# Kernel tuning notes

Measured on AMD Instinct MI355X. Metric: run time of the kernel, lower is better.

## Reference

```python
import jax, jax.numpy as jnp
import numpy as np

B, S, DMAX, NMEL, DM, K = 8, 100, 12, 80, 128, 9
T = S * DMAX  # 1200 max mel frames
EPS = 1e-5  # BatchNorm eps (eval mode, running_mean=0, running_var=1)


def setup_inputs() -> dict:
    key = jax.random.key(0)
    ks = jax.random.split(key, 16)
    durations = jax.random.randint(ks[0], (B, S), 4, DMAX + 1).astype(jnp.int32)
    mel_len = jnp.sum(durations, axis=1).astype(jnp.int32)
    src_len = jnp.full((B,), S, dtype=jnp.int32)
    mel = jax.random.normal(ks[1], (B, T, NMEL), dtype=jnp.float32)
    # conv stack params (xavier-ish uniform)
    s1 = float(np.sqrt(6.0 / (1 * K + DM * K)))
    w1 = jax.random.uniform(ks[2], (DM, 1, 1, K), minval=-s1, maxval=s1, dtype=jnp.float32)
    g1 = 1.0 + 0.1 * jax.random.normal(ks[3], (DM,), dtype=jnp.float32)
    be1 = 0.1 * jax.random.normal(ks[4], (DM,), dtype=jnp.float32)
    s2 = float(np.sqrt(6.0 / (DM * K + 1 * K)))
    w2 = jax.random.uniform(ks[5], (1, DM, 1, K), minval=-s2, maxval=s2, dtype=jnp.float32)
    g2 = 1.0 + 0.1 * jax.random.normal(ks[6], (1,), dtype=jnp.float32)
    be2 = 0.1 * jax.random.normal(ks[7], (1,), dtype=jnp.float32)
    # BiGRU params (pytorch layout: gates [r|z|n] stacked -> 3*H rows)
    sh = float(1.0 / np.sqrt(DM))
    u = lambda k, shape: jax.random.uniform(k, shape, minval=-sh, maxval=sh, dtype=jnp.float32)
    w_ih_f = u(ks[8], (3 * DM, NMEL)); w_hh_f = u(ks[9], (3 * DM, DM))
    b_ih_f = u(ks[10], (3 * DM,));    b_hh_f = u(ks[11], (3 * DM,))
    w_ih_b = u(ks[12], (3 * DM, NMEL)); w_hh_b = u(ks[13], (3 * DM, DM))
    b_ih_b = u(ks[14], (3 * DM,));    b_hh_b = u(ks[15], (3 * DM,))
    return {"mel": mel, "durations": durations, "mel_len": mel_len, "src_len": src_len,
            "w1": w1, "g1": g1, "be1": be1, "w2": w2, "g2": g2, "be2": be2,
            "w_ih_f": w_ih_f, "w_hh_f": w_hh_f, "b_ih_f": b_ih_f, "b_hh_f": b_hh_f,
            "w_ih_b": w_ih_b, "w_hh_b": w_hh_b, "b_ih_b": b_ih_b, "b_hh_b": b_hh_b}


def _bn_eval(x, g, b):
    # eval-mode BatchNorm2d with running_mean=0, running_var=1; x [B,C,T,M]
    scale = g / jnp.sqrt(1.0 + EPS)
    return x * scale[None, :, None, None] + b[None, :, None, None]


def _gru_scan(xs_seq, reset_seq, w_hh, b_hh):
    # xs_seq [T,B,3H] precomputed input projections; reset_seq [T,B] 1.0 -> reset h to 0
    H = w_hh.shape[1]
    Bn = xs_seq.shape[1]

    def step(h, inp):
        xg, rst = inp
        h = h * (1.0 - rst)[:, None]
        hg = h @ w_hh.T + b_hh
        xr, xz, xn = jnp.split(xg, 3, axis=-1)
        hr, hz, hn = jnp.split(hg, 3, axis=-1)
        r = jax.nn.sigmoid(xr + hr)
        z = jax.nn.sigmoid(xz + hz)
        n = jnp.tanh(xn + r * hn)
        h_new = (1.0 - z) * n + z * h
        return h_new, h_new

    h0 = jnp.zeros((Bn, H), xs_seq.dtype)
    _, hs = jax.lax.scan(step, h0, (xs_seq, reset_seq))
    return hs  # [T,B,H]


def reference(mel, durations, mel_len, src_len, w1, g1, be1, w2, g2, be2,
              w_ih_f, w_hh_f, b_ih_f, b_hh_f, w_ih_b, w_hh_b, b_ih_b, b_hh_b):
    pad = (K - 1) // 2
    # conv stack: kernel (1,K) mixes only the mel-channel axis -> apply to full mel once
    x = mel[:, None, :, :]  # [B,1,T,M]
    x = jax.lax.conv_general_dilated(x, w1, (1, 1), [(0, 0), (pad, pad)])
    x = jax.nn.relu(_bn_eval(x, g1, be1))
    x = jax.lax.conv_general_dilated(x, w2, (1, 1), [(0, 0), (pad, pad)])
    x = jax.nn.relu(_bn_eval(x, g2, be2))
    x = x[:, 0]  # [B,T,M]

    # segment boundaries from durations (all phones valid here, durations > 0)
    cum = jnp.cumsum(durations, axis=1)      # [B,S]
    starts = cum - durations                 # segment start frame per phone
    ends = cum - 1                           # segment end frame per phone
    bidx = jnp.arange(B)[:, None]
    start_mask = jnp.zeros((B, T), x.dtype).at[bidx, starts].set(1.0)
    end_mask = jnp.zeros((B, T), x.dtype).at[bidx, ends].set(1.0)

    # forward direction: reset h at segment starts, read h at segment ends
    xf = jnp.einsum('btm,gm->tbg', x, w_ih_f) + b_ih_f
    Hf = _gru_scan(xf, start_mask.T, w_hh_f, b_hh_f)           # [T,B,H]
    # backward direction: scan reversed time, reset at original segment ends
    xb = jnp.einsum('btm,gm->tbg', x, w_ih_b) + b_ih_b
    Hb = _gru_scan(xb[::-1], end_mask.T[::-1], w_hh_b, b_hh_b)[::-1]  # [T,B,H], orig time

    hf = jnp.take_along_axis(jnp.transpose(Hf, (1, 0, 2)), ends[..., None], axis=1)    # [B,S,H]
    hb = jnp.take_along_axis(jnp.transpose(Hb, (1, 0, 2)), starts[..., None], axis=1)  # [B,S,H]
    out = jnp.concatenate([hf, hb], axis=-1)  # [B,S,2H]
    valid = (jnp.arange(S)[None, :] < src_len[:, None])[..., None]
    return jnp.where(valid, out, 0.0)
```

## Files before the change

kernel.cpp:

```cpp
#include <hip/hip_runtime.h>
#include <math.h>

#define BB   8
#define SS   100
#define TT   1200
#define NM   80
#define DMC  128
#define KK   9
#define G3   384
#define NROW (BB*TT)

typedef __attribute__((ext_vector_type(8))) short short8;
typedef __attribute__((ext_vector_type(4))) float f32x4;

__device__ __forceinline__ float sigmoid_(float v) { return 1.f / (1.f + __expf(-v)); }
__device__ __forceinline__ float tanh_(float v) {
    float a = fabsf(v);
    float e = __expf(-2.f * a);
    float t = (1.f - e) / (1.f + e);
    return copysignf(t, v);
}
__device__ __forceinline__ unsigned short f2bf(float f) {
    unsigned int u = __float_as_uint(f);
    unsigned int r = (u + 0x7fffu + ((u >> 16) & 1u)) >> 16;
    return (unsigned short)r;
}

__global__ __launch_bounds__(1024) void k_prep(
    const float* __restrict__ whf, const float* __restrict__ whb,
    const float* __restrict__ wif, const float* __restrict__ wib,
    const float* __restrict__ bf, const float* __restrict__ bbv,
    const int* __restrict__ dur,
    unsigned short* __restrict__ wph, unsigned short* __restrict__ wpl,
    unsigned short* __restrict__ wih_h, unsigned short* __restrict__ wih_l,
    float* __restrict__ biasc, int* __restrict__ starts) {
    int blk = blockIdx.x;
    int tid = threadIdx.x;
    if (blk < 12) {
        int idx = blk * 1024 + tid;
        int lane = idx & 63;
        int k32  = (idx >> 6) & 3;
        int tau  = (idx >> 8) % 24;
        int dir  = idx / (24 * 4 * 64);
        const float* w = dir ? whb : whf;
        int g = tau * 16 + (lane & 15);
        int kbase = k32 * 32 + (lane >> 4) * 8;
#pragma unroll
        for (int j = 0; j < 8; j++) {
            float v = w[g * DMC + kbase + j];
            unsigned short hi = f2bf(v);
            float hif = __uint_as_float(((unsigned)hi) << 16);
            unsigned short lo = f2bf(v - hif);
            wph[idx * 8 + j] = hi;
            wpl[idx * 8 + j] = lo;
        }
    } else if (blk < 21) {
        int idx = (blk - 12) * 1024 + tid;
        int lane = idx & 63;
        int ks   = (idx >> 6) % 3;
        int tau  = idx / (3 * 64);
        int gate = tau * 16 + (lane & 15);
        int kb   = ks * 32 + (lane >> 4) * 8;
        const float* w = (gate < G3) ? (wif + gate * NM) : (wib + (gate - G3) * NM);
#pragma unroll
        for (int j = 0; j < 8; j++) {
            int k = kb + j;
            float v = (k < NM) ? w[k] : 0.f;
            unsigned short hi = f2bf(v);
            float hif = __uint_as_float(((unsigned)hi) << 16);
            unsigned short lo = f2bf(v - hif);
            wih_h[idx * 8 + j] = hi;
            wih_l[idx * 8 + j] = lo;
        }
    } else {
        __shared__ int buf[BB][128];
        int s = tid & 127, b = tid >> 7;
        int v = (s < SS) ? dur[b * SS + s] : 0;
        buf[b][s] = v;
        __syncthreads();
        for (int off = 1; off < 128; off <<= 1) {
            int t = (s >= off) ? buf[b][s - off] : 0;
            __syncthreads();
            buf[b][s] += t;
            __syncthreads();
        }
        if (s < SS) starts[b * SS + s] = buf[b][s] - v;
        if (tid < 768) biasc[tid] = (tid < G3) ? bf[tid] : bbv[tid - G3];
    }
}

__global__ __launch_bounds__(256) void k_conv(
    const float* __restrict__ mel, const int* __restrict__ mel_len,
    const float* __restrict__ w1, const float* __restrict__ g1, const float* __restrict__ be1,
    const float* __restrict__ w2, const float* __restrict__ g2, const float* __restrict__ be2,
    float* __restrict__ xout) {
    int b = blockIdx.y;
    int t = blockIdx.x;
    int ml = mel_len[b];
    if (t >= ml) return;

    __shared__ __align__(16) float mp[96];
    __shared__ __align__(16) float part[8][84];

    int tid = threadIdx.x;
    int mq = tid >> 6, g = tid & 63;
    int ms = 20 * mq;
    const float inv_sqrt = 0.9999950000374997f;

    if (tid < 96) {
        float v = 0.f;
        if (tid >= 8 && tid < 88) v = mel[(b * TT + t) * NM + tid - 8];
        mp[tid] = v;
    }
    __syncthreads();

    float c[20];
#pragma unroll
    for (int m = 0; m < 20; m++) c[m] = 0.f;

#pragma unroll 1
    for (int dd = 0; dd < 2; dd++) {
        int d = g + 64 * dd;
        float sc = g1[d] * inv_sqrt;
        float w1r[KK], w2r[KK];
#pragma unroll
        for (int k = 0; k < KK; k++) { w1r[k] = w1[d * KK + k] * sc; w2r[k] = w2[d * KK + k]; }
        float sb = be1[d];

        float mw[12];
        {
            const float4* p4 = (const float4*)(mp + ms);
            float4 a = p4[0], bq = p4[1], cq = p4[2];
            mw[0]=a.x;  mw[1]=a.y;  mw[2]=a.z;  mw[3]=a.w;
            mw[4]=bq.x; mw[5]=bq.y; mw[6]=bq.z; mw[7]=bq.w;
            mw[8]=cq.x; mw[9]=cq.y; mw[10]=cq.z; mw[11]=cq.w;
        }
#pragma unroll
        for (int ch = 0; ch < 7; ch++) {
#pragma unroll
            for (int jj = 0; jj < 4; jj++) {
                int off = ch * 4 + jj;
                float yv = sb;
#pragma unroll
                for (int k = 0; k < KK; k++) yv = fmaf(w1r[k], mw[jj + k], yv);
                yv = fmaxf(yv, 0.f);
                int j = ms + off;
                if (j < 4 || j >= 84) yv = 0.f;
#pragma unroll
                for (int k = 0; k < KK; k++) {
                    int mo = off - k;
                    if (mo >= 0 && mo < 20) c[mo] = fmaf(w2r[k], yv, c[mo]);
                }
            }
            if (ch < 6) {
#pragma unroll
                for (int q = 0; q < 8; q++) mw[q] = mw[q + 4];
                const float4* p4 = (const float4*)(mp + ms + ch * 4 + 12);
                float4 a = p4[0];
                mw[8]=a.x; mw[9]=a.y; mw[10]=a.z; mw[11]=a.w;
            }
        }
    }

#pragma unroll
    for (int m = 0; m < 20; m++) {
        c[m] += __shfl_xor(c[m], 1);
        c[m] += __shfl_xor(c[m], 2);
        c[m] += __shfl_xor(c[m], 4);
    }
    if ((g & 7) == 0) {
        int p = g >> 3;
#pragma unroll
        for (int m = 0; m < 20; m += 4)
            *(float4*)&part[p][ms + m] = make_float4(c[m], c[m+1], c[m+2], c[m+3]);
    }
    __syncthreads();

    if (tid < 80) {
        float s = 0.f;
#pragma unroll
        for (int p = 0; p < 8; p++) s += part[p][tid];
        float v = fmaxf(0.f, fmaf(s, g2[0] * inv_sqrt, be2[0]));
        xout[(b * TT + t) * NM + tid] = v;
    }
}

__global__ __launch_bounds__(512, 2) void k_gru(
    const float* __restrict__ x,
    const unsigned short* __restrict__ wph, const unsigned short* __restrict__ wpl,
    const unsigned short* __restrict__ wih_h, const unsigned short* __restrict__ wih_l,
    const float* __restrict__ biasc,
    const int* __restrict__ dur_all, const int* __restrict__ starts,
    const int* __restrict__ src_len,
    const float* __restrict__ bhf, const float* __restrict__ bhb,
    float* __restrict__ out) {
    int sblk = blockIdx.x;
    int b    = blockIdx.y;
    int dir  = blockIdx.z;
    int s0 = sblk * 16;

    __shared__ __align__(16) unsigned short hbh[2][2048];
    __shared__ __align__(16) unsigned short hbl[2][2048];
    __shared__ __align__(16) short8 xbh[2][192];
    __shared__ __align__(16) short8 xbl[2][192];
    __shared__ int sdur[16], sstart[16];

    int tid  = threadIdx.x;
    int wave = tid >> 6, lane = tid & 63;
    int quad = lane >> 4, seg = lane & 15;

    if (tid < 16) {
        int ss = s0 + tid;
        sdur[tid]   = (ss < SS) ? dur_all[b * SS + ss] : 0;
        sstart[tid] = (ss < SS) ? starts[b * SS + ss]  : 0;
    }
    for (int i = tid; i < 2048; i += 512) { hbh[0][i] = 0; hbl[0][i] = 0; }

    short8 Ah[3][4], Al[3][4];
    const short8* wph8 = (const short8*)wph;
    const short8* wpl8 = (const short8*)wpl;
#pragma unroll
    for (int tt = 0; tt < 3; tt++)
#pragma unroll
        for (int k32 = 0; k32 < 4; k32++) {
            int idx = ((dir * 24 + wave + 8 * tt) * 4 + k32) * 64 + lane;
            Ah[tt][k32] = wph8[idx];
            Al[tt][k32] = wpl8[idx];
        }
    short8 Gh[3][3], Gl[3][3];
    const short8* wih_h8 = (const short8*)wih_h;
    const short8* wih_l8 = (const short8*)wih_l;
#pragma unroll
    for (int tt = 0; tt < 3; tt++)
#pragma unroll
        for (int ks = 0; ks < 3; ks++) {
            int idx = ((dir * 24 + wave + 8 * tt) * 3 + ks) * 64 + lane;
            Gh[tt][ks] = wih_h8[idx];
            Gl[tt][ks] = wih_l8[idx];
        }

    int s = s0 + seg;
    int sd = (s < SS) ? dur_all[b * SS + s] : 0;
    int st = (s < SS) ? starts[b * SS + s]  : 0;
    int slb = src_len[b];
    const float* bih = biasc + dir * G3;
    const float* bhh = dir ? bhb : bhf;
    int j0 = wave * 16 + quad * 4;
    float4 i_r = *(const float4*)&bih[j0];
    float4 i_z = *(const float4*)&bih[DMC + j0];
    float4 bxn = *(const float4*)&bih[2 * DMC + j0];
    float4 h_r = *(const float4*)&bhh[j0];
    float4 h_z = *(const float4*)&bhh[DMC + j0];
    float4 bhn = *(const float4*)&bhh[2 * DMC + j0];
    float4 br = make_float4(i_r.x + h_r.x, i_r.y + h_r.y, i_r.z + h_r.z, i_r.w + h_r.w);
    float4 bz = make_float4(i_z.x + h_z.x, i_z.y + h_z.y, i_z.z + h_z.z, i_z.w + h_z.w);
    float4 h = make_float4(0.f, 0.f, 0.f, 0.f);

    int idx8 = (j0 >> 5) * 64 + ((j0 >> 3) & 3) * 16 + seg;
    int wbase = idx8 * 8 + (j0 & 7);

    __syncthreads();

    if (tid < 192) {
        int ks = tid >> 6, ln = tid & 63;
        int sg = ln & 15, qq = ln >> 4;
        int kb = ks * 32 + qq * 8;
        short8 hi8 = {0,0,0,0,0,0,0,0}, lo8 = {0,0,0,0,0,0,0,0};
        if (kb < NM && 0 < sdur[sg]) {
            int t = dir ? (sstart[sg] + sdur[sg] - 1) : sstart[sg];
            const float* xr = x + (size_t)(b * TT + t) * NM + kb;
#pragma unroll
            for (int j = 0; j < 8; j++) {
                float v = xr[j];
                unsigned short hi = f2bf(v);
                hi8[j] = (short)hi;
                lo8[j] = (short)f2bf(v - __uint_as_float(((unsigned)hi) << 16));
            }
        }
        xbh[0][tid] = hi8;
        xbl[0][tid] = lo8;
    }
    __syncthreads();

    for (int i = 0; i < 12; i++) {
        int p = i & 1;
        bool act = (i < sd);

        f32x4 acc0 = (f32x4){0.f,0.f,0.f,0.f};
        f32x4 acc1 = (f32x4){0.f,0.f,0.f,0.f};
        f32x4 acc2 = (f32x4){0.f,0.f,0.f,0.f};
        f32x4 acc3 = (f32x4){0.f,0.f,0.f,0.f};
#pragma unroll
        for (int ks = 0; ks < 3; ks++) {
            short8 Bxh = xbh[p][ks * 64 + lane];
            short8 Bxl = xbl[p][ks * 64 + lane];
            acc0 = __builtin_amdgcn_mfma_f32_16x16x32_bf16(Gh[0][ks], Bxh, acc0, 0, 0, 0);
            acc0 = __builtin_amdgcn_mfma_f32_16x16x32_bf16(Gh[0][ks], Bxl, acc0, 0, 0, 0);
            acc0 = __builtin_amdgcn_mfma_f32_16x16x32_bf16(Gl[0][ks], Bxh, acc0, 0, 0, 0);
            acc1 = __builtin_amdgcn_mfma_f32_16x16x32_bf16(Gh[1][ks], Bxh, acc1, 0, 0, 0);
            acc1 = __builtin_amdgcn_mfma_f32_16x16x32_bf16(Gh[1][ks], Bxl, acc1, 0, 0, 0);
            acc1 = __builtin_amdgcn_mfma_f32_16x16x32_bf16(Gl[1][ks], Bxh, acc1, 0, 0, 0);
            acc3 = __builtin_amdgcn_mfma_f32_16x16x32_bf16(Gh[2][ks], Bxh, acc3, 0, 0, 0);
            acc3 = __builtin_amdgcn_mfma_f32_16x16x32_bf16(Gh[2][ks], Bxl, acc3, 0, 0, 0);
            acc3 = __builtin_amdgcn_mfma_f32_16x16x32_bf16(Gl[2][ks], Bxh, acc3, 0, 0, 0);
        }
#pragma unroll
        for (int k32 = 0; k32 < 4; k32++) {
            short8 Bh = ((const short8*)hbh[p])[k32 * 64 + lane];
            short8 Bl = ((const short8*)hbl[p])[k32 * 64 + lane];
            acc0 = __builtin_amdgcn_mfma_f32_16x16x32_bf16(Ah[0][k32], Bh, acc0, 0, 0, 0);
            acc0 = __builtin_amdgcn_mfma_f32_16x16x32_bf16(Ah[0][k32], Bl, acc0, 0, 0, 0);
            acc0 = __builtin_amdgcn_mfma_f32_16x16x32_bf16(Al[0][k32], Bh, acc0, 0, 0, 0);
            acc1 = __builtin_amdgcn_mfma_f32_16x16x32_bf16(Ah[1][k32], Bh, acc1, 0, 0, 0);
            acc1 = __builtin_amdgcn_mfma_f32_16x16x32_bf16(Ah[1][k32], Bl, acc1, 0, 0, 0);
            acc1 = __builtin_amdgcn_mfma_f32_16x16x32_bf16(Al[1][k32], Bh, acc1, 0, 0, 0);
            acc2 = __builtin_amdgcn_mfma_f32_16x16x32_bf16(Ah[2][k32], Bh, acc2, 0, 0, 0);
            acc2 = __builtin_amdgcn_mfma_f32_16x16x32_bf16(Ah[2][k32], Bl, acc2, 0, 0, 0);
            acc2 = __builtin_amdgcn_mfma_f32_16x16x32_bf16(Al[2][k32], Bh, acc2, 0, 0, 0);
        }

        if (act) {
            float hv[4]  = {h.x, h.y, h.z, h.w};
            float brv[4] = {br.x, br.y, br.z, br.w};
            float bzv[4] = {bz.x, bz.y, bz.z, bz.w};
            float bxv[4] = {bxn.x, bxn.y, bxn.z, bxn.w};
            float bhv[4] = {bhn.x, bhn.y, bhn.z, bhn.w};
#pragma unroll
            for (int cmp = 0; cmp < 4; cmp++) {
                float r = sigmoid_(acc0[cmp] + brv[cmp]);
                float z = sigmoid_(acc1[cmp] + bzv[cmp]);
                float n = tanh_(acc3[cmp] + bxv[cmp] + r * (acc2[cmp] + bhv[cmp]));
                hv[cmp] = (1.f - z) * n + z * hv[cmp];
            }
            h = make_float4(hv[0], hv[1], hv[2], hv[3]);
            if (i == sd - 1) {
                float4 vout = (s < slb) ? h : make_float4(0.f, 0.f, 0.f, 0.f);
                *(float4*)&out[(b * SS + s) * (2 * DMC) + dir * DMC + j0] = vout;
            }
        }

        {
            float hv[4] = {h.x, h.y, h.z, h.w};
            unsigned short hs_[4], ls_[4];
#pragma unroll
            for (int cmp = 0; cmp < 4; cmp++) {
                unsigned short hi = f2bf(hv[cmp]);
                float hif = __uint_as_float(((unsigned)hi) << 16);
                hs_[cmp] = hi;
                ls_[cmp] = f2bf(hv[cmp] - hif);
            }
            *(ushort4*)&hbh[1 - p][wbase] = make_ushort4(hs_[0], hs_[1], hs_[2], hs_[3]);
            *(ushort4*)&hbl[1 - p][wbase] = make_ushort4(ls_[0], ls_[1], ls_[2], ls_[3]);
        }

        if (tid < 192) {
            int i2 = i + 1;
            int ks = tid >> 6, ln = tid & 63;
            int sg = ln & 15, qq = ln >> 4;
            int kb = ks * 32 + qq * 8;
            short8 hi8 = {0,0,0,0,0,0,0,0}, lo8 = {0,0,0,0,0,0,0,0};
            int d2 = sdur[sg];
            if (kb < NM && i2 < d2) {
                int t = dir ? (sstart[sg] + d2 - 1 - i2) : (sstart[sg] + i2);
                const float* xr = x + (size_t)(b * TT + t) * NM + kb;
#pragma unroll
                for (int j = 0; j < 8; j++) {
                    float v = xr[j];
                    unsigned short hi = f2bf(v);
                    hi8[j] = (short)hi;
                    lo8[j] = (short)f2bf(v - __uint_as_float(((unsigned)hi) << 16));
                }
            }
            xbh[1 - p][tid] = hi8;
            xbl[1 - p][tid] = lo8;
        }
        __syncthreads();
    }
}

extern "C" void kernel_launch(void* const* d_in, const int* in_sizes, int n_in,
                              void* d_out, int out_size, void* d_ws, size_t ws_size,
                              hipStream_t stream) {
    const float* mel      = (const float*)d_in[0];
    const int*   durations= (const int*)  d_in[1];
    const int*   mel_len  = (const int*)  d_in[2];
    const int*   src_len  = (const int*)  d_in[3];
    const float* w1       = (const float*)d_in[4];
    const float* g1       = (const float*)d_in[5];
    const float* be1      = (const float*)d_in[6];
    const float* w2       = (const float*)d_in[7];
    const float* g2       = (const float*)d_in[8];
    const float* be2      = (const float*)d_in[9];
    const float* w_ih_f   = (const float*)d_in[10];
    const float* w_hh_f   = (const float*)d_in[11];
    const float* b_ih_f   = (const float*)d_in[12];
    const float* b_hh_f   = (const float*)d_in[13];
    const float* w_ih_b   = (const float*)d_in[14];
    const float* w_hh_b   = (const float*)d_in[15];
    const float* b_ih_b   = (const float*)d_in[16];
    const float* b_hh_b   = (const float*)d_in[17];
    float* out = (float*)d_out;

    float* x    = (float*)d_ws;
    unsigned short* wph   = (unsigned short*)(x + NROW * NM);
    unsigned short* wpl   = wph + 2 * 24 * 4 * 64 * 8;
    unsigned short* wih_h = wpl + 2 * 24 * 4 * 64 * 8;
    unsigned short* wih_l = wih_h + 48 * 3 * 64 * 8;
    float* biasc = (float*)(wih_l + 48 * 3 * 64 * 8);
    int*   starts= (int*)(biasc + 768);

    k_prep<<<22, 1024, 0, stream>>>(w_hh_f, w_hh_b, w_ih_f, w_ih_b, b_ih_f, b_ih_b,
                                    durations, wph, wpl, wih_h, wih_l, biasc, starts);
    k_conv<<<dim3(TT, BB), 256, 0, stream>>>(mel, mel_len, w1, g1, be1, w2, g2, be2, x);
    k_gru<<<dim3(7, 8, 2), 512, 0, stream>>>(x, wph, wpl, wih_h, wih_l, biasc,
                                             durations, starts, src_len,
                                             b_hh_f, b_hh_b, out);
}
```

Measured before the change: 166.9 us.

## Pair conv frames with packed FMA and preload all GRU inputs upfront

The conv kernel now handles two time frames per block and uses v_pk_fma_f32 on interleaved float pairs, which halves the block count and shares weight loads between the two frames. The GRU kernel now converts all 12 steps' input vectors to bf16 hi/lo in shared memory before the recurrence starts. This removes the per-step global load and conversion from the serial loop. The x and h projections also go into separate accumulators, which shortens the MFMA dependency chains. The cost is more shared memory per GRU block, which may lower occupancy, and a longer prologue.

```diff
diff --git a/kernel.cpp b/kernel.cpp
--- a/kernel.cpp
+++ b/kernel.cpp
@@ -12,6 +12,7 @@
 
 typedef __attribute__((ext_vector_type(8))) short short8;
 typedef __attribute__((ext_vector_type(4))) float f32x4;
+typedef __attribute__((ext_vector_type(2))) float f32x2;
 
 __device__ __forceinline__ float sigmoid_(float v) { return 1.f / (1.f + __expf(-v)); }
 __device__ __forceinline__ float tanh_(float v) {
@@ -24,6 +25,11 @@
     unsigned int u = __float_as_uint(f);
     unsigned int r = (u + 0x7fffu + ((u >> 16) & 1u)) >> 16;
     return (unsigned short)r;
+}
+__device__ __forceinline__ f32x2 pk_fma(f32x2 a, f32x2 b, f32x2 c) {
+    f32x2 d;
+    asm("v_pk_fma_f32 %0, %1, %2, %3" : "=v"(d) : "v"(a), "v"(b), "v"(c));
+    return d;
 }
 
 __global__ __launch_bounds__(1024) void k_prep(
@@ -94,94 +100,113 @@
     const float* __restrict__ w1, const float* __restrict__ g1, const float* __restrict__ be1,
     const float* __restrict__ w2, const float* __restrict__ g2, const float* __restrict__ be2,
     float* __restrict__ xout) {
-    int b = blockIdx.y;
-    int t = blockIdx.x;
+    int b  = blockIdx.y;
+    int t0 = blockIdx.x * 2;
     int ml = mel_len[b];
-    if (t >= ml) return;
-
-    __shared__ __align__(16) float mp[96];
-    __shared__ __align__(16) float part[8][84];
+    if (t0 >= ml) return;
+
+    __shared__ __align__(16) f32x2 mp2[96];
+    __shared__ __align__(16) f32x2 part2[8][82];
 
     int tid = threadIdx.x;
     int mq = tid >> 6, g = tid & 63;
     int ms = 20 * mq;
     const float inv_sqrt = 0.9999950000374997f;
 
-    if (tid < 96) {
+    if (tid < 192) {
+        int rr = tid / 96, i = tid - rr * 96;
         float v = 0.f;
-        if (tid >= 8 && tid < 88) v = mel[(b * TT + t) * NM + tid - 8];
-        mp[tid] = v;
+        if (i >= 8 && i < 88) v = mel[(b * TT + t0 + rr) * NM + i - 8];
+        ((float*)mp2)[i * 2 + rr] = v;
     }
     __syncthreads();
 
-    float c[20];
-#pragma unroll
-    for (int m = 0; m < 20; m++) c[m] = 0.f;
+    f32x2 c[20];
+#pragma unroll
+    for (int m = 0; m < 20; m++) c[m] = (f32x2){0.f, 0.f};
 
 #pragma unroll 1
     for (int dd = 0; dd < 2; dd++) {
         int d = g + 64 * dd;
         float sc = g1[d] * inv_sqrt;
-        float w1r[KK], w2r[KK];
-#pragma unroll
-        for (int k = 0; k < KK; k++) { w1r[k] = w1[d * KK + k] * sc; w2r[k] = w2[d * KK + k]; }
+        f32x2 w1p[KK], w2p[KK];
+#pragma unroll
+        for (int k = 0; k < KK; k++) {
+            float a = w1[d * KK + k] * sc;
+            float bq = w2[d * KK + k];
+            w1p[k] = (f32x2){a, a};
+            w2p[k] = (f32x2){bq, bq};
+        }
         float sb = be1[d];
 
-        float mw[12];
+        f32x2 mw[12];
         {
-            const float4* p4 = (const float4*)(mp + ms);
-            float4 a = p4[0], bq = p4[1], cq = p4[2];
-            mw[0]=a.x;  mw[1]=a.y;  mw[2]=a.z;  mw[3]=a.w;
-            mw[4]=bq.x; mw[5]=bq.y; mw[6]=bq.z; mw[7]=bq.w;
-            mw[8]=cq.x; mw[9]=cq.y; mw[10]=cq.z; mw[11]=cq.w;
+            const float4* p4 = (const float4*)(mp2 + ms);
+#pragma unroll
+            for (int q = 0; q < 6; q++) {
+                float4 v = p4[q];
+                mw[2 * q]     = (f32x2){v.x, v.y};
+                mw[2 * q + 1] = (f32x2){v.z, v.w};
+            }
         }
 #pragma unroll
         for (int ch = 0; ch < 7; ch++) {
 #pragma unroll
             for (int jj = 0; jj < 4; jj++) {
                 int off = ch * 4 + jj;
-                float yv = sb;
-#pragma unroll
-                for (int k = 0; k < KK; k++) yv = fmaf(w1r[k], mw[jj + k], yv);
-                yv = fmaxf(yv, 0.f);
+                f32x2 yv = (f32x2){sb, sb};
+#pragma unroll
+                for (int k = 0; k < KK; k++) yv = pk_fma(w1p[k], mw[jj + k], yv);
+                yv[0] = fmaxf(yv[0], 0.f);
+                yv[1] = fmaxf(yv[1], 0.f);
                 int j = ms + off;
-                if (j < 4 || j >= 84) yv = 0.f;
+                if (j < 4 || j >= 84) yv = (f32x2){0.f, 0.f};
 #pragma unroll
                 for (int k = 0; k < KK; k++) {
                     int mo = off - k;
-                    if (mo >= 0 && mo < 20) c[mo] = fmaf(w2r[k], yv, c[mo]);
+                    if (mo >= 0 && mo < 20) c[mo] = pk_fma(w2p[k], yv, c[mo]);
                 }
             }
             if (ch < 6) {
 #pragma unroll
                 for (int q = 0; q < 8; q++) mw[q] = mw[q + 4];
-                const float4* p4 = (const float4*)(mp + ms + ch * 4 + 12);
-                float4 a = p4[0];
-                mw[8]=a.x; mw[9]=a.y; mw[10]=a.z; mw[11]=a.w;
+                const float4* p4 = (const float4*)(mp2 + ms + ch * 4 + 12);
+                float4 a0 = p4[0], a1 = p4[1];
+                mw[8]  = (f32x2){a0.x, a0.y};
+                mw[9]  = (f32x2){a0.z, a0.w};
+                mw[10] = (f32x2){a1.x, a1.y};
+                mw[11] = (f32x2){a1.z, a1.w};
             }
         }
     }
 
 #pragma unroll
     for (int m = 0; m < 20; m++) {
-        c[m] += __shfl_xor(c[m], 1);
-        c[m] += __shfl_xor(c[m], 2);
-        c[m] += __shfl_xor(c[m], 4);
+        c[m][0] += __shfl_xor(c[m][0], 1);
+        c[m][1] += __shfl_xor(c[m][1], 1);
+        c[m][0] += __shfl_xor(c[m][0], 2);
+        c[m][1] += __shfl_xor(c[m][1], 2);
+        c[m][0] += __shfl_xor(c[m][0], 4);
+        c[m][1] += __shfl_xor(c[m][1], 4);
     }
     if ((g & 7) == 0) {
         int p = g >> 3;
 #pragma unroll
-        for (int m = 0; m < 20; m += 4)
-            *(float4*)&part[p][ms + m] = make_float4(c[m], c[m+1], c[m+2], c[m+3]);
+        for (int m = 0; m < 20; m++) part2[p][ms + m] = c[m];
     }
     __syncthreads();
 
-    if (tid < 80) {
-        float s = 0.f;
-#pragma unroll
-        for (int p = 0; p < 8; p++) s += part[p][tid];
-        float v = fmaxf(0.f, fmaf(s, g2[0] * inv_sqrt, be2[0]));
-        xout[(b * TT + t) * NM + tid] = v;
+    if (tid < 160) {
+        int rr = (tid >= 80) ? 1 : 0;
+        int m  = tid - 80 * rr;
+        int t  = t0 + rr;
+        if (t < ml) {
+            float s = 0.f;
+#pragma unroll
+            for (int p = 0; p < 8; p++) s += part2[p][m][rr];
+            float v = fmaxf(0.f, fmaf(s, g2[0] * inv_sqrt, be2[0]));
+            xout[(b * TT + t) * NM + m] = v;
+        }
     }
 }
 
@@ -199,10 +224,10 @@
     int dir  = blockIdx.z;
     int s0 = sblk * 16;
 
+    __shared__ __align__(16) short8 xbh[12][192];
+    __shared__ __align__(16) short8 xbl[12][192];
     __shared__ __align__(16) unsigned short hbh[2][2048];
     __shared__ __align__(16) unsigned short hbl[2][2048];
-    __shared__ __align__(16) short8 xbh[2][192];
-    __shared__ __align__(16) short8 xbl[2][192];
     __shared__ int sdur[16], sstart[16];
 
     int tid  = threadIdx.x;
@@ -241,7 +266,6 @@
 
     int s = s0 + seg;
     int sd = (s < SS) ? dur_all[b * SS + s] : 0;
-    int st = (s < SS) ? starts[b * SS + s]  : 0;
     int slb = src_len[b];
     const float* bih = biasc + dir * G3;
     const float* bhh = dir ? bhb : bhf;
@@ -261,24 +285,31 @@
 
     __syncthreads();
 
-    if (tid < 192) {
-        int ks = tid >> 6, ln = tid & 63;
-        int sg = ln & 15, qq = ln >> 4;
-        int kb = ks * 32 + qq * 8;
-        short8 hi8 = {0,0,0,0,0,0,0,0}, lo8 = {0,0,0,0,0,0,0,0};
-        if (kb < NM && 0 < sdur[sg]) {
-            int t = dir ? (sstart[sg] + sdur[sg] - 1) : sstart[sg];
-            const float* xr = x + (size_t)(b * TT + t) * NM + kb;
-#pragma unroll
-            for (int j = 0; j < 8; j++) {
-                float v = xr[j];
-                unsigned short hi = f2bf(v);
-                hi8[j] = (short)hi;
-                lo8[j] = (short)f2bf(v - __uint_as_float(((unsigned)hi) << 16));
-            }
-        }
-        xbh[0][tid] = hi8;
-        xbl[0][tid] = lo8;
+#pragma unroll
+    for (int q = 0; q < 5; q++) {
+        int u = tid + q * 512;
+        if (u < 12 * 192) {
+            int it  = u / 192;
+            int rem = u - it * 192;
+            int ks = rem >> 6, ln = rem & 63;
+            int sg = ln & 15, qq = ln >> 4;
+            int kb = ks * 32 + qq * 8;
+            short8 hi8 = {0,0,0,0,0,0,0,0}, lo8 = {0,0,0,0,0,0,0,0};
+            int d2 = sdur[sg];
+            if (kb < NM && it < d2) {
+                int t = dir ? (sstart[sg] + d2 - 1 - it) : (sstart[sg] + it);
+                const float* xr = x + (size_t)(b * TT + t) * NM + kb;
+#pragma unroll
+                for (int j = 0; j < 8; j++) {
+                    float v = xr[j];
+                    unsigned short hi = f2bf(v);
+                    hi8[j] = (short)hi;
+                    lo8[j] = (short)f2bf(v - __uint_as_float(((unsigned)hi) << 16));
+                }
+            }
+            xbh[it][rem] = hi8;
+            xbl[it][rem] = lo8;
+        }
     }
     __syncthreads();
 
@@ -286,37 +317,39 @@
         int p = i & 1;
         bool act = (i < sd);
 
-        f32x4 acc0 = (f32x4){0.f,0.f,0.f,0.f};
-        f32x4 acc1 = (f32x4){0.f,0.f,0.f,0.f};
-        f32x4 acc2 = (f32x4){0.f,0.f,0.f,0.f};
-        f32x4 acc3 = (f32x4){0.f,0.f,0.f,0.f};
+        f32x4 axr = (f32x4){0.f,0.f,0.f,0.f};
+        f32x4 axz = (f32x4){0.f,0.f,0.f,0.f};
+        f32x4 axn = (f32x4){0.f,0.f,0.f,0.f};
+        f32x4 ahr = (f32x4){0.f,0.f,0.f,0.f};
+        f32x4 ahz = (f32x4){0.f,0.f,0.f,0.f};
+        f32x4 ahn = (f32x4){0.f,0.f,0.f,0.f};
 #pragma unroll
         for (int ks = 0; ks < 3; ks++) {
-            short8 Bxh = xbh[p][ks * 64 + lane];
-            short8 Bxl = xbl[p][ks * 64 + lane];
-            acc0 = __builtin_amdgcn_mfma_f32_16x16x32_bf16(Gh[0][ks], Bxh, acc0, 0, 0, 0);
-            acc0 = __builtin_amdgcn_mfma_f32_16x16x32_bf16(Gh[0][ks], Bxl, acc0, 0, 0, 0);
-            acc0 = __builtin_amdgcn_mfma_f32_16x16x32_bf16(Gl[0][ks], Bxh, acc0, 0, 0, 0);
-            acc1 = __builtin_amdgcn_mfma_f32_16x16x32_bf16(Gh[1][ks], Bxh, acc1, 0, 0, 0);
-            acc1 = __builtin_amdgcn_mfma_f32_16x16x32_bf16(Gh[1][ks], Bxl, acc1, 0, 0, 0);
-            acc1 = __builtin_amdgcn_mfma_f32_16x16x32_bf16(Gl[1][ks], Bxh, acc1, 0, 0, 0);
-            acc3 = __builtin_amdgcn_mfma_f32_16x16x32_bf16(Gh[2][ks], Bxh, acc3, 0, 0, 0);
-            acc3 = __builtin_amdgcn_mfma_f32_16x16x32_bf16(Gh[2][ks], Bxl, acc3, 0, 0, 0);
-            acc3 = __builtin_amdgcn_mfma_f32_16x16x32_bf16(Gl[2][ks], Bxh, acc3, 0, 0, 0);
+            short8 Bxh = xbh[i][ks * 64 + lane];
+            short8 Bxl = xbl[i][ks * 64 + lane];
+            axr = __builtin_amdgcn_mfma_f32_16x16x32_bf16(Gh[0][ks], Bxh, axr, 0, 0, 0);
+            axr = __builtin_amdgcn_mfma_f32_16x16x32_bf16(Gh[0][ks], Bxl, axr, 0, 0, 0);
+            axr = __builtin_amdgcn_mfma_f32_16x16x32_bf16(Gl[0][ks], Bxh, axr, 0, 0, 0);
+            axz = __builtin_amdgcn_mfma_f32_16x16x32_bf16(Gh[1][ks], Bxh, axz, 0, 0, 0);
+            axz = __builtin_amdgcn_mfma_f32_16x16x32_bf16(Gh[1][ks], Bxl, axz, 0, 0, 0);
+            axz = __builtin_amdgcn_mfma_f32_16x16x32_bf16(Gl[1][ks], Bxh, axz, 0, 0, 0);
+            axn = __builtin_amdgcn_mfma_f32_16x16x32_bf16(Gh[2][ks], Bxh, axn, 0, 0, 0);
+            axn = __builtin_amdgcn_mfma_f32_16x16x32_bf16(Gh[2][ks], Bxl, axn, 0, 0, 0);
+            axn = __builtin_amdgcn_mfma_f32_16x16x32_bf16(Gl[2][ks], Bxh, axn, 0, 0, 0);
         }
 #pragma unroll
         for (int k32 = 0; k32 < 4; k32++) {
             short8 Bh = ((const short8*)hbh[p])[k32 * 64 + lane];
             short8 Bl = ((const short8*)hbl[p])[k32 * 64 + lane];
-            acc0 = __builtin_amdgcn_mfma_f32_16x16x32_bf16(Ah[0][k32], Bh, acc0, 0, 0, 0);
-            acc0 = __builtin_amdgcn_mfma_f32_16x16x32_bf16(Ah[0][k32], Bl, acc0, 0, 0, 0);
-            acc0 = __builtin_amdgcn_mfma_f32_16x16x32_bf16(Al[0][k32], Bh, acc0, 0, 0, 0);
-            acc1 = __builtin_amdgcn_mfma_f32_16x16x32_bf16(Ah[1][k32], Bh, acc1, 0, 0, 0);
-            acc1 = __builtin_amdgcn_mfma_f32_16x16x32_bf16(Ah[1][k32], Bl, acc1, 0, 0, 0);
-            acc1 = __builtin_amdgcn_mfma_f32_16x16x32_bf16(Al[1][k32], Bh, acc1, 0, 0, 0);
-            acc2 = __builtin_amdgcn_mfma_f32_16x16x32_bf16(Ah[2][k32], Bh, acc2, 0, 0, 0);
-            acc2 = __builtin_amdgcn_mfma_f32_16x16x32_bf16(Ah[2][k32], Bl, acc2, 0, 0, 0);
-            acc2 = __builtin_amdgcn_mfma_f32_16x16x32_bf16(Al[2][k32], Bh, acc2, 0, 0, 0);
+            ahr = __builtin_amdgcn_mfma_f32_16x16x32_bf16(Ah[0][k32], Bh, ahr, 0, 0, 0);
+            ahr = __builtin_amdgcn_mfma_f32_16x16x32_bf16(Ah[0][k32], Bl, ahr, 0, 0, 0);
+            ahr = __builtin_amdgcn_mfma_f32_16x16x32_bf16(Al[0][k32], Bh, ahr, 0, 0, 0);
+            ahz = __builtin_amdgcn_mfma_f32_16x16x32_bf16(Ah[1][k32], Bh, ahz, 0, 0, 0);
+            ahz = __builtin_amdgcn_mfma_f32_16x16x32_bf16(Ah[1][k32], Bl, ahz, 0, 0, 0);
+            ahz = __builtin_amdgcn_mfma_f32_16x16x32_bf16(Al[1][k32], Bh, ahz, 0, 0, 0);
+            ahn = __builtin_amdgcn_mfma_f32_16x16x32_bf16(Ah[2][k32], Bh, ahn, 0, 0, 0);
+            ahn = __builtin_amdgcn_mfma_f32_16x16x32_bf16(Ah[2][k32], Bl, ahn, 0, 0, 0);
+            ahn = __builtin_amdgcn_mfma_f32_16x16x32_bf16(Al[2][k32], Bh, ahn, 0, 0, 0);
         }
 
         if (act) {
@@ -327,9 +360,9 @@
             float bhv[4] = {bhn.x, bhn.y, bhn.z, bhn.w};
 #pragma unroll
             for (int cmp = 0; cmp < 4; cmp++) {
-                float r = sigmoid_(acc0[cmp] + brv[cmp]);
-                float z = sigmoid_(acc1[cmp] + bzv[cmp]);
-                float n = tanh_(acc3[cmp] + bxv[cmp] + r * (acc2[cmp] + bhv[cmp]));
+                float r = sigmoid_(axr[cmp] + ahr[cmp] + brv[cmp]);
+                float z = sigmoid_(axz[cmp] + ahz[cmp] + bzv[cmp]);
+                float n = tanh_(axn[cmp] + bxv[cmp] + r * (ahn[cmp] + bhv[cmp]));
                 hv[cmp] = (1.f - z) * n + z * hv[cmp];
             }
             h = make_float4(hv[0], hv[1], hv[2], hv[3]);
@@ -351,28 +384,6 @@
             }
             *(ushort4*)&hbh[1 - p][wbase] = make_ushort4(hs_[0], hs_[1], hs_[2], hs_[3]);
             *(ushort4*)&hbl[1 - p][wbase] = make_ushort4(ls_[0], ls_[1], ls_[2], ls_[3]);
-        }
-
-        if (tid < 192) {
-            int i2 = i + 1;
-            int ks = tid >> 6, ln = tid & 63;
-            int sg = ln & 15, qq = ln >> 4;
-            int kb = ks * 32 + qq * 8;
-            short8 hi8 = {0,0,0,0,0,0,0,0}, lo8 = {0,0,0,0,0,0,0,0};
-            int d2 = sdur[sg];
-            if (kb < NM && i2 < d2) {
-                int t = dir ? (sstart[sg] + d2 - 1 - i2) : (sstart[sg] + i2);
-                const float* xr = x + (size_t)(b * TT + t) * NM + kb;
-#pragma unroll
-                for (int j = 0; j < 8; j++) {
-                    float v = xr[j];
-                    unsigned short hi = f2bf(v);
-                    hi8[j] = (short)hi;
-                    lo8[j] = (short)f2bf(v - __uint_as_float(((unsigned)hi) << 16));
-                }
-            }
-            xbh[1 - p][tid] = hi8;
-            xbl[1 - p][tid] = lo8;
         }
         __syncthreads();
     }
@@ -411,7 +422,7 @@
 
     k_prep<<<22, 1024, 0, stream>>>(w_hh_f, w_hh_b, w_ih_f, w_ih_b, b_ih_f, b_ih_b,
                                     durations, wph, wpl, wih_h, wih_l, biasc, starts);
-    k_conv<<<dim3(TT, BB), 256, 0, stream>>>(mel, mel_len, w1, g1, be1, w2, g2, be2, x);
+    k_conv<<<dim3(TT / 2, BB), 256, 0, stream>>>(mel, mel_len, w1, g1, be1, w2, g2, be2, x);
     k_gru<<<dim3(7, 8, 2), 512, 0, stream>>>(x, wph, wpl, wih_h, wih_l, biasc,
                                              durations, starts, src_len,
                                              b_hh_f, b_hh_b, out);
```

After: 165.8 us. Within noise of the previous version (-0.7%).
